# Kernel tuning notes

Measured on AMD Instinct MI355X. Metric: run time of the kernel, lower is better.

The kernel has to match this reference:

```python
import jax, jax.numpy as jnp
import numpy as np

B, N, M = 4, 1024, 3072          # batch, latent (query) len, prefix context len
D, H, DH, L, F = 512, 8, 64, 6, 2048  # dim, heads, dim_head, depth, ff hidden
SCALE = DH ** -0.5


def _ln(x, g, b):
    m = jnp.mean(x, axis=-1, keepdims=True)
    v = jnp.mean(jnp.square(x - m), axis=-1, keepdims=True)
    return (x - m) * jax.lax.rsqrt(v + 1e-5) * g + b


def _heads(t):  # [b, n, h*d] -> [b, h, n, d]
    b, n, _ = t.shape
    return t.reshape(b, n, H, DH).transpose(0, 2, 1, 3)


def _attend(q, k, v):
    # q:[b,h,i,d], k/v:[b,h,j,d]; causal mask triu(j-i+1) as in source
    i, j = q.shape[2], k.shape[2]
    sim = jnp.einsum('bhid,bhjd->bhij', q * SCALE, k)
    mask = jnp.triu(jnp.ones((i, j), dtype=bool), j - i + 1)
    sim = jnp.where(mask, -jnp.finfo(sim.dtype).max, sim)
    attn = jax.nn.softmax(sim, axis=-1)
    out = jnp.einsum('bhij,bhjd->bhid', attn, v)
    return out.transpose(0, 2, 1, 3).reshape(q.shape[0], i, H * DH)


def _ff(x, g, b, w1, w2):
    return jax.nn.gelu(_ln(x, g, b) @ w1, approximate=False) @ w2


def setup_inputs() -> dict:
    key = jax.random.key(0)
    ks = jax.random.split(key, 12)
    rn = lambda k, shape: jax.random.normal(k, shape, dtype=jnp.float32) * 0.02
    return {
        'x': jax.random.normal(ks[0], (B, N, D), jnp.float32),
        'context': jax.random.normal(ks[1], (B, M, D), jnp.float32),
        'pa_norm_g': jnp.ones((D,), jnp.float32), 'pa_norm_b': jnp.zeros((D,), jnp.float32),
        'pa_cnorm_g': jnp.ones((D,), jnp.float32), 'pa_cnorm_b': jnp.zeros((D,), jnp.float32),
        'pa_wq': rn(ks[2], (D, H * DH)), 'pa_wkv': rn(ks[3], (D, 2 * H * DH)),
        'pa_wo': rn(ks[4], (H * DH, D)), 'pa_wo_b': jnp.zeros((D,), jnp.float32),
        'pf_ln_g': jnp.ones((D,), jnp.float32), 'pf_ln_b': jnp.zeros((D,), jnp.float32),
        'pf_w1': rn(ks[5], (D, F)), 'pf_w2': rn(ks[6], (F, D)),
        'sa_ln_g': jnp.ones((L, D), jnp.float32), 'sa_ln_b': jnp.zeros((L, D), jnp.float32),
        'sa_wqkv': rn(ks[7], (L, D, 3 * H * DH)), 'sa_wo': rn(ks[8], (L, H * DH, D)),
        'sf_ln_g': jnp.ones((L, D), jnp.float32), 'sf_ln_b': jnp.zeros((L, D), jnp.float32),
        'sf_w1': rn(ks[9], (L, D, F)), 'sf_w2': rn(ks[10], (L, F, D)),
    }


def reference(x, context, pa_norm_g, pa_norm_b, pa_cnorm_g, pa_cnorm_b,
              pa_wq, pa_wkv, pa_wo, pa_wo_b, pf_ln_g, pf_ln_b, pf_w1, pf_w2,
              sa_ln_g, sa_ln_b, sa_wqkv, sa_wo, sf_ln_g, sf_ln_b, sf_w1, sf_w2):
    # --- CausalPrefixAttention (eval mode: no dropout, context_mask=None) ---
    xn = _ln(x, pa_norm_g, pa_norm_b)
    cn = _ln(context, pa_cnorm_g, pa_cnorm_b)
    q = _heads(xn @ pa_wq)
    k_in, v_in = jnp.split(xn @ pa_wkv, 2, axis=-1)
    k_c, v_c = jnp.split(cn @ pa_wkv, 2, axis=-1)
    k = _heads(jnp.concatenate([k_c, k_in], axis=1))  # [b,h,M+N,d]
    v = _heads(jnp.concatenate([v_c, v_in], axis=1))
    x = _attend(q, k, v) @ pa_wo + pa_wo_b + x
    x = _ff(x, pf_ln_g, pf_ln_b, pf_w1, pf_w2) + x
    # --- depth x (CausalAttention + FeedForward) ---
    for l in range(L):
        xn = _ln(x, sa_ln_g[l], sa_ln_b[l])
        qq, kk, vv = jnp.split(xn @ sa_wqkv[l], 3, axis=-1)
        x = _attend(_heads(qq), _heads(kk), _heads(vv)) @ sa_wo[l] + x
        x = _ff(x, sf_ln_g[l], sf_ln_b[l], sf_w1[l], sf_w2[l]) + x
    return x
```

## Files before the change

kernel.cpp:

```cpp
#include <hip/hip_runtime.h>
#include <hip/hip_bf16.h>
#include <cstdint>
#include <cstddef>

typedef __bf16 bf16;
typedef __attribute__((ext_vector_type(8))) __bf16 bf16x8;
typedef __attribute__((ext_vector_type(4))) __bf16 bf16x4;
typedef __attribute__((ext_vector_type(4))) float f32x4;

constexpr int B_ = 4, QN = 1024, MCTX = 3072, D_ = 512, H_ = 8, DHE = 64, L_ = 6, FF_ = 2048;
constexpr float SCL2_ = 0.18033688011f;

__device__ __forceinline__ f32x4 mfma16(bf16x8 a, bf16x8 b, f32x4 c) {
  return __builtin_amdgcn_mfma_f32_16x16x32_bf16(a, b, c, 0, 0, 0);
}

__device__ __forceinline__ void gl_lds16(const bf16* g, bf16* l) {
  __builtin_amdgcn_global_load_lds((const __attribute__((address_space(1))) void*)g,
                                   (__attribute__((address_space(3))) void*)l, 16, 0, 0);
}

__device__ __forceinline__ float fexp2(float x) {
  float r;
  asm("v_exp_f32 %0, %1" : "=v"(r) : "v"(x));
  return r;
}

__global__ __launch_bounds__(256) void ln_kernel(const float* __restrict__ x,
                                                 const float* __restrict__ g,
                                                 const float* __restrict__ b,
                                                 bf16* __restrict__ out, int rows) {
  int wid = threadIdx.x >> 6, lane = threadIdx.x & 63;
  int row = blockIdx.x * 4 + wid;
  if (row >= rows) return;
  const float* xr = x + (size_t)row * D_;
  f32x4 a0 = *(const f32x4*)(xr + lane * 8);
  f32x4 a1 = *(const f32x4*)(xr + lane * 8 + 4);
  float s = 0.f;
#pragma unroll
  for (int i = 0; i < 4; i++) { s += a0[i]; s += a1[i]; }
#pragma unroll
  for (int d = 1; d < 64; d <<= 1) s += __shfl_xor(s, d);
  float mean = s * (1.0f / 512.0f);
  float q = 0.f;
#pragma unroll
  for (int i = 0; i < 4; i++) {
    float t0 = a0[i] - mean, t1 = a1[i] - mean;
    q += t0 * t0 + t1 * t1;
  }
#pragma unroll
  for (int d = 1; d < 64; d <<= 1) q += __shfl_xor(q, d);
  float rstd = rsqrtf(q * (1.0f / 512.0f) + 1e-5f);
  f32x4 g0 = *(const f32x4*)(g + lane * 8);
  f32x4 g1 = *(const f32x4*)(g + lane * 8 + 4);
  f32x4 b0 = *(const f32x4*)(b + lane * 8);
  f32x4 b1 = *(const f32x4*)(b + lane * 8 + 4);
  bf16x8 o;
#pragma unroll
  for (int i = 0; i < 4; i++) {
    o[i] = (bf16)((a0[i] - mean) * rstd * g0[i] + b0[i]);
    o[i + 4] = (bf16)((a1[i] - mean) * rstd * g1[i] + b1[i]);
  }
  *(bf16x8*)(out + (size_t)row * D_ + lane * 8) = o;
}

struct WDesc { const float* src; bf16* dst; int K; int N; int tstart; };
struct WPack { WDesc d[30]; int n; };

__global__ __launch_bounds__(256) void wtrans_all(WPack p) {
  __shared__ float tile[64][65];
  const int bid = blockIdx.x;
  int mi = 0;
  for (int i = 1; i < p.n; i++)
    if (p.d[i].tstart <= bid) mi = i;
  const float* src = p.d[mi].src;
  bf16* dst = p.d[mi].dst;
  const int K = p.d[mi].K, N = p.d[mi].N;
  const int lt = bid - p.d[mi].tstart;
  const int ntx = N >> 6;
  const int n0 = (lt % ntx) * 64, k0 = (lt / ntx) * 64;
  const int tx = threadIdx.x, ty = threadIdx.y;
#pragma unroll
  for (int pp = 0; pp < 16; pp++)
    tile[pp * 4 + ty][tx] = src[(size_t)(k0 + pp * 4 + ty) * N + n0 + tx];
  __syncthreads();
#pragma unroll
  for (int pp = 0; pp < 16; pp++)
    dst[(size_t)(n0 + pp * 4 + ty) * K + k0 + tx] = (bf16)tile[tx][pp * 4 + ty];
}

template <int EPI>
__global__ __launch_bounds__(256) void gemm128(const bf16* __restrict__ A,
                                               const bf16* __restrict__ BT,
                                               void* __restrict__ C0,
                                               void* __restrict__ C1,
                                               void* __restrict__ C2,
                                               const float* __restrict__ resid,
                                               const float* __restrict__ bias,
                                               int M, int N, int K, int vstr) {
  __shared__ bf16 sm[6 * 4096];
  bf16* sA = sm;
  bf16* sB = sm + 3 * 4096;
  const int tid = threadIdx.x, wid = tid >> 6, lane = tid & 63;
  const int lr = lane & 15, lg = lane >> 4;
  const int tm = blockIdx.y * 128, tn = blockIdx.x * 128;
  const int wr = (wid >> 1) * 64, wc = (wid & 1) * 64;

  const int r0 = tid >> 2, ls0 = tid & 3;
  const int gs0 = ls0 ^ (r0 & 3);
  const bf16* gA0 = A + (size_t)(tm + r0) * K + gs0 * 8;
  const bf16* gB0 = BT + (size_t)(tn + r0) * K + gs0 * 8;
  const bf16* gA1 = gA0 + (size_t)64 * K;
  const bf16* gB1 = gB0 + (size_t)64 * K;

  f32x4 acc[4][4] = {};
  const int nt = K >> 5;

  auto stage = [&](int bi, int kt) {
    gl_lds16(gA0 + kt, sA + bi * 4096 + tid * 8);
    gl_lds16(gA1 + kt, sA + bi * 4096 + (tid + 256) * 8);
    gl_lds16(gB0 + kt, sB + bi * 4096 + tid * 8);
    gl_lds16(gB1 + kt, sB + bi * 4096 + (tid + 256) * 8);
  };

  stage(0, 0);
  stage(1, 32);

  for (int t = 0; t < nt; ++t) {
    const int bi = t % 3;
    if (t + 1 < nt) {
      asm volatile("s_waitcnt vmcnt(4)" ::: "memory");
    } else {
      asm volatile("s_waitcnt vmcnt(0)" ::: "memory");
    }
    __builtin_amdgcn_s_barrier();
    __builtin_amdgcn_sched_barrier(0);
    if (t + 2 < nt) stage((t + 2) % 3, (t + 2) * 32);

    bf16x8 af[4], bfr[4];
#pragma unroll
    for (int i = 0; i < 4; i++) {
      const int row = wr + i * 16 + lr;
      af[i] = *(const bf16x8*)&sA[bi * 4096 + row * 32 + ((lg ^ (row & 3)) * 8)];
    }
#pragma unroll
    for (int j = 0; j < 4; j++) {
      const int row = wc + j * 16 + lr;
      bfr[j] = *(const bf16x8*)&sB[bi * 4096 + row * 32 + ((lg ^ (row & 3)) * 8)];
    }
#pragma unroll
    for (int i = 0; i < 4; i++)
#pragma unroll
      for (int j = 0; j < 4; j++)
        acc[i][j] = mfma16(af[i], bfr[j], acc[i][j]);
  }

  const bool row_major_dst =
      (EPI == 1) || (EPI == 3 && tn < 1024) || (EPI == 4 && tn < 1024) || (EPI == 5 && tn < 512);
  if (row_major_dst) {
    bf16* dst;
    int dstr, rbase, coff;
    if (EPI == 1) { dst = (bf16*)C0; dstr = N; rbase = tm; coff = tn; }
    else if (EPI == 3) {
      if (tn < 512) { dst = (bf16*)C0; dstr = 512; rbase = tm; coff = tn; }
      else { dst = (bf16*)C1; dstr = 1024; rbase = (tm >> 10) * 4096 + (tm & 1023) + 3072; coff = tn - 512; }
    } else if (EPI == 4) { dst = (bf16*)C0; dstr = 1536; rbase = tm; coff = tn; }
    else { dst = (bf16*)C1; dstr = 1024; rbase = (tm / 3072) * 4096 + (tm % 3072); coff = tn; }

    __syncthreads();
    bf16* lb = sm;
#pragma unroll
    for (int i = 0; i < 4; i++) {
#pragma unroll
      for (int r = 0; r < 4; r++) {
        const int row = wr + i * 16 + lg * 4 + r;
#pragma unroll
        for (int j = 0; j < 4; j++) {
          const int col = wc + j * 16 + lr;
          float v = acc[i][j][r];
          if (EPI == 1) {
            float u = v * (0.7978845608f + 0.0356774081f * v * v);
            float e = fexp2(fminf(2.885390082f * u, 80.0f));
            v = v * e / (1.0f + e);
          }
          lb[row * 128 + (col ^ ((row & 7) << 3))] = (bf16)v;
        }
      }
    }
    __syncthreads();
#pragma unroll
    for (int p = 0; p < 8; p++) {
      const int row = p * 16 + (tid >> 4);
      const int cb = (tid & 15) * 8;
      bf16x8 v = *(const bf16x8*)&lb[row * 128 + (cb ^ ((row & 7) << 3))];
      *(bf16x8*)&dst[(size_t)(rbase + row) * dstr + coff + cb] = v;
    }
  } else {
#pragma unroll
    for (int i = 0; i < 4; i++) {
      const int row = tm + wr + i * 16 + lg * 4;
#pragma unroll
      for (int j = 0; j < 4; j++) {
        const int col = tn + wc + j * 16 + lr;
        bf16x4 pk = {(bf16)acc[i][j][0], (bf16)acc[i][j][1],
                     (bf16)acc[i][j][2], (bf16)acc[i][j][3]};
        if (EPI == 3) {
          const int cc = col - 1024, hh = cc >> 6, dh = cc & 63;
          const int bb = row >> 10, s = (row & 1023) + 3072;
          *(bf16x4*)&((bf16*)C2)[((size_t)(bb * 8 + hh) * 64 + dh) * vstr + s] = pk;
        } else if (EPI == 4) {
          const int cc = col - 1024, hh = cc >> 6, dh = cc & 63;
          const int bb = row >> 10, s = row & 1023;
          *(bf16x4*)&((bf16*)C2)[((size_t)(bb * 8 + hh) * 64 + dh) * vstr + s] = pk;
        } else {
          const int bq = row / 3072, s = row - bq * 3072;
          const int cc = col - 512, hh = cc >> 6, dh = cc & 63;
          *(bf16x4*)&((bf16*)C2)[((size_t)(bq * 8 + hh) * 64 + dh) * vstr + s] = pk;
        }
      }
    }
  }
}

__global__ __launch_bounds__(512) void gemm64k2(const bf16* __restrict__ A,
                                                const bf16* __restrict__ BT,
                                                float* __restrict__ Cout,
                                                const float* __restrict__ resid,
                                                const float* __restrict__ bias,
                                                int M, int N, int K) {
  __shared__ bf16 sm[3][2][64 * 64];
  const int tid = threadIdx.x, wid = tid >> 6, lane = tid & 63;
  const int lr = lane & 15, lg = lane >> 4;
  const int tm = blockIdx.y * 64, tn = blockIdx.x * 64;
  const int ws = wid >> 2;
  const int wq = wid & 3;
  const int wr = (wq >> 1) * 32, wc = (wq & 1) * 32;

  const int r0 = tid >> 3, u0 = tid & 7;
  const int g0 = u0 ^ (r0 & 7);
  const bf16* gA0 = A + (size_t)(tm + r0) * K + g0 * 8;
  const bf16* gB0 = BT + (size_t)(tn + r0) * K + g0 * 8;

  auto stage = [&](int bi, int kt) {
    gl_lds16(gA0 + kt, &sm[bi][0][tid * 8]);
    gl_lds16(gB0 + kt, &sm[bi][1][tid * 8]);
  };

  f32x4 acc[2][2] = {};
  const int nt = K >> 6;
  stage(0, 0);
  if (nt > 1) stage(1, 64);

  for (int t = 0; t < nt; ++t) {
    const int bi = t % 3;
    if (t + 1 < nt) {
      asm volatile("s_waitcnt vmcnt(2)" ::: "memory");
    } else {
      asm volatile("s_waitcnt vmcnt(0)" ::: "memory");
    }
    __builtin_amdgcn_s_barrier();
    __builtin_amdgcn_sched_barrier(0);
    if (t + 2 < nt) stage((t + 2) % 3, (t + 2) * 64);

    bf16x8 af[2], bfr[2];
#pragma unroll
    for (int i = 0; i < 2; i++) {
      const int row = wr + i * 16 + lr;
      af[i] = *(const bf16x8*)&sm[bi][0][row * 64 + (((ws * 4 + lg) ^ (row & 7)) * 8)];
    }
#pragma unroll
    for (int j = 0; j < 2; j++) {
      const int row = wc + j * 16 + lr;
      bfr[j] = *(const bf16x8*)&sm[bi][1][row * 64 + (((ws * 4 + lg) ^ (row & 7)) * 8)];
    }
#pragma unroll
    for (int i = 0; i < 2; i++)
#pragma unroll
      for (int j = 0; j < 2; j++)
        acc[i][j] = mfma16(af[i], bfr[j], acc[i][j]);
  }

  __syncthreads();
  float* lbuf = (float*)&sm[0][0][0];
  if (ws == 0) {
#pragma unroll
    for (int i = 0; i < 2; i++)
#pragma unroll
      for (int r = 0; r < 4; r++) {
        const int row = wr + i * 16 + lg * 4 + r;
#pragma unroll
        for (int j = 0; j < 2; j++)
          lbuf[row * 68 + wc + j * 16 + lr] = acc[i][j][r];
      }
  }
  __syncthreads();
  if (ws == 1) {
#pragma unroll
    for (int i = 0; i < 2; i++)
#pragma unroll
      for (int r = 0; r < 4; r++) {
        const int row = wr + i * 16 + lg * 4 + r;
#pragma unroll
        for (int j = 0; j < 2; j++)
          lbuf[row * 68 + wc + j * 16 + lr] += acc[i][j][r];
      }
  }
  __syncthreads();
#pragma unroll
  for (int p = 0; p < 2; p++) {
    const int row = p * 32 + (tid >> 4);
    const int col = (tid & 15) * 4;
    f32x4 v = *(const f32x4*)&lbuf[row * 68 + col];
    const size_t gidx = (size_t)(tm + row) * N + tn + col;
    f32x4 rs = *(const f32x4*)&resid[gidx];
    if (bias) {
      f32x4 bs = *(const f32x4*)&bias[tn + col];
#pragma unroll
      for (int e = 0; e < 4; e++) v[e] += bs[e];
    }
#pragma unroll
    for (int e = 0; e < 4; e++) v[e] += rs[e];
    *(f32x4*)&Cout[gidx] = v;
  }
}

template <int NSPLIT>
__global__ __launch_bounds__(512) void attn_kernel(const bf16* __restrict__ q, int qstride,
                                                   const bf16* __restrict__ k, int kstride,
                                                   const bf16* __restrict__ vt,
                                                   bf16* __restrict__ out,
                                                   bf16* __restrict__ po,
                                                   float* __restrict__ pm,
                                                   float* __restrict__ pl,
                                                   int Skv, int Moff, int spllen) {
  __shared__ bf16 kls[2][4096];
  __shared__ bf16 vls[2][4096];
  __shared__ bf16 pls[8][1024];

  const int tid = threadIdx.x, wid = tid >> 6, lane = tid & 63;
  const int lr = lane & 15, lg = lane >> 4, lg4 = lg * 4;
  const int b = blockIdx.z, h = blockIdx.y;
  const int qblk = blockIdx.x / NSPLIT;
  const int split = blockIdx.x % NSPLIT;
  const int q0b = qblk * 128;
  const int q0w = q0b + wid * 16;
  const int kv_lo = split * spllen;

  int jhi_blk = Moff + q0b + 127;
  if (jhi_blk > Skv - 1) jhi_blk = Skv - 1;
  int hi = kv_lo + spllen;
  if (hi > jhi_blk + 1) hi = jhi_blk + 1;
  const int ntl = (hi > kv_lo) ? ((hi - kv_lo + 63) >> 6) : 0;

  if (NSPLIT > 1 && ntl == 0) {
    size_t rb = ((size_t)split * B_ * H_ + (size_t)b * H_ + h) * QN + q0w;
    const int row = lane >> 2;
    bf16x8 z = {};
#pragma unroll
    for (int half = 0; half < 2; half++)
      *(bf16x8*)&po[(rb + row) * 64 + (lane & 3) * 16 + half * 8] = z;
    if (lg == 0) { pm[rb + lr] = -3e38f; pl[rb + lr] = 0.f; }
    return;
  }

  const int sel = ((tid >> 6) & 1) * 32 + ((tid >> 4) & 3) * 8;
  const int srow0 = (tid >> 7) * 16 + (tid & 15);
  const bf16* kbase = k + (size_t)b * Skv * kstride + h * DHE + sel;
  const bf16* vbase = vt + (size_t)((b * H_ + h) * DHE) * Skv + sel;

  const bf16* qp = q + (size_t)(b * QN + q0w + lr) * qstride + h * DHE;
  bf16x8 qa0 = *(const bf16x8*)(qp + lg * 8);
  bf16x8 qa1 = *(const bf16x8*)(qp + 32 + lg * 8);
#pragma unroll
  for (int i = 0; i < 8; i++) {
    qa0[i] = (bf16)((float)qa0[i] * SCL2_);
    qa1[i] = (bf16)((float)qa1[i] * SCL2_);
  }
  bf16x8 vones;
#pragma unroll
  for (int i = 0; i < 8; i++) vones[i] = (bf16)1.0f;

  f32x4 o[4] = {};
  f32x4 o4 = {};

  auto stage = [&](int bi, int j0) {
    gl_lds16(kbase + (size_t)(j0 + srow0) * kstride, &kls[bi][tid * 8]);
    gl_lds16(vbase + (size_t)srow0 * Skv + j0, &vls[bi][tid * 8]);
  };

  stage(0, kv_lo);
  __syncthreads();
  int buf = 0;
  bf16* pw = &pls[wid][0];

  for (int t = 0; t < ntl; ++t) {
    const int j0 = kv_lo + t * 64;
    if (t + 1 < ntl) stage(buf ^ 1, j0 + 64);
    const bf16* kbp = &kls[buf][0];
    const bf16* vbp = &vls[buf][0];

    f32x4 sv[4];
    __builtin_amdgcn_s_setprio(1);
#pragma unroll
    for (int kg = 0; kg < 4; kg++) {
      bf16x8 k0 = *(const bf16x8*)(kbp + (kg * 128 + lane) * 8);
      bf16x8 k1 = *(const bf16x8*)(kbp + (kg * 128 + 64 + lane) * 8);
      f32x4 z = {0.f, 0.f, 0.f, 0.f};
      z = mfma16(k0, qa0, z);
      z = mfma16(k1, qa1, z);
      sv[kg] = z;
    }
    __builtin_amdgcn_s_setprio(0);
    const bool full = (j0 + 63 <= Moff + q0w);
    if (!full) {
      const int limq = Moff + q0w + lr;
#pragma unroll
      for (int kg = 0; kg < 4; kg++)
#pragma unroll
        for (int r = 0; r < 4; r++)
          if (j0 + kg * 16 + lg4 + r > limq) sv[kg][r] = -3e38f;
    }
#pragma unroll
    for (int kg = 0; kg < 4; kg++) {
      float p0 = fexp2(sv[kg][0]);
      float p1 = fexp2(sv[kg][1]);
      float p2 = fexp2(sv[kg][2]);
      float p3 = fexp2(sv[kg][3]);
      bf16x4 pk = {(bf16)p0, (bf16)p1, (bf16)p2, (bf16)p3};
      const int k8 = kg * 2 + (lg >> 1);
      *(bf16x4*)(pw + ((k8 >> 2) * 64 + (k8 & 3) * 16 + lr) * 8 + (lg & 1) * 4) = pk;
    }
    bf16x8 pa0 = *(const bf16x8*)(pw + lane * 8);
    bf16x8 pa1 = *(const bf16x8*)(pw + (64 + lane) * 8);
    __builtin_amdgcn_s_setprio(1);
#pragma unroll
    for (int f = 0; f < 4; f++) {
      bf16x8 v0 = *(const bf16x8*)(vbp + (f * 128 + lane) * 8);
      bf16x8 v1 = *(const bf16x8*)(vbp + (f * 128 + 64 + lane) * 8);
      o[f] = mfma16(pa0, v0, o[f]);
      o[f] = mfma16(pa1, v1, o[f]);
    }
    o4 = mfma16(pa0, vones, o4);
    o4 = mfma16(pa1, vones, o4);
    __builtin_amdgcn_s_setprio(0);
    __syncthreads();
    buf ^= 1;
  }

  if (NSPLIT == 1) {
    float li[4];
#pragma unroll
    for (int r = 0; r < 4; r++) li[r] = 1.0f / o4[r];
#pragma unroll
    for (int f = 0; f < 4; f++)
#pragma unroll
      for (int r = 0; r < 4; r++) {
        const int row = lg4 + r, col = f * 16 + lr;
        pw[row * 64 + (col ^ ((row & 7) << 3))] = (bf16)(o[f][r] * li[r]);
      }
    const int row = lane >> 2;
#pragma unroll
    for (int half = 0; half < 2; half++) {
      const int cb = (lane & 3) * 16 + half * 8;
      bf16x8 v = *(const bf16x8*)&pw[row * 64 + (cb ^ ((row & 7) << 3))];
      *(bf16x8*)&out[(size_t)(b * QN + q0w + row) * D_ + h * DHE + cb] = v;
    }
  } else {
    size_t rb = ((size_t)split * B_ * H_ + (size_t)b * H_ + h) * QN + q0w;
#pragma unroll
    for (int f = 0; f < 4; f++)
#pragma unroll
      for (int r = 0; r < 4; r++) {
        const int row = lg4 + r, col = f * 16 + lr;
        pw[row * 64 + (col ^ ((row & 7) << 3))] = (bf16)o[f][r];
      }
    const int row = lane >> 2;
#pragma unroll
    for (int half = 0; half < 2; half++) {
      const int cb = (lane & 3) * 16 + half * 8;
      bf16x8 v = *(const bf16x8*)&pw[row * 64 + (cb ^ ((row & 7) << 3))];
      *(bf16x8*)&po[(rb + row) * 64 + cb] = v;
    }
    if (lr == 0) {
#pragma unroll
      for (int r = 0; r < 4; r++) {
        pm[rb + lg4 + r] = 0.f;
        pl[rb + lg4 + r] = o4[r];
      }
    }
  }
}

template <int NSPLIT>
__global__ __launch_bounds__(256) void attn_combine(const bf16* __restrict__ po,
                                                    const float* __restrict__ pm,
                                                    const float* __restrict__ pl,
                                                    bf16* __restrict__ out) {
  constexpr int TOT = B_ * H_ * QN;
  const int wid = threadIdx.x >> 6, lane = threadIdx.x & 63;
  const int row = blockIdx.x * 4 + wid;
  float mv[NSPLIT], lv[NSPLIT];
  float mstar = -3e38f;
#pragma unroll
  for (int s = 0; s < NSPLIT; s++) {
    mv[s] = pm[s * TOT + row];
    lv[s] = pl[s * TOT + row];
    mstar = fmaxf(mstar, mv[s]);
  }
  float lstar = 0.f, acc = 0.f;
#pragma unroll
  for (int s = 0; s < NSPLIT; s++) {
    float w = fexp2(mv[s] - mstar);
    lstar += lv[s] * w;
    acc += (float)po[((size_t)s * TOT + row) * 64 + lane] * w;
  }
  const int b = row >> 13, hq = row & 8191, h = hq >> 10, qq = hq & 1023;
  out[((size_t)b * QN + qq) * D_ + h * DHE + lane] = (bf16)(acc / lstar);
}

extern "C" void kernel_launch(void* const* d_in, const int* in_sizes, int n_in,
                              void* d_out, int out_size, void* d_ws, size_t ws_size,
                              hipStream_t stream) {
  const float* x       = (const float*)d_in[0];
  const float* ctx     = (const float*)d_in[1];
  const float* pa_ng   = (const float*)d_in[2];
  const float* pa_nb   = (const float*)d_in[3];
  const float* pa_cg   = (const float*)d_in[4];
  const float* pa_cb   = (const float*)d_in[5];
  const float* pa_wq   = (const float*)d_in[6];
  const float* pa_wkv  = (const float*)d_in[7];
  const float* pa_wo   = (const float*)d_in[8];
  const float* pa_wob  = (const float*)d_in[9];
  const float* pf_g    = (const float*)d_in[10];
  const float* pf_b    = (const float*)d_in[11];
  const float* pf_w1   = (const float*)d_in[12];
  const float* pf_w2   = (const float*)d_in[13];
  const float* sa_g    = (const float*)d_in[14];
  const float* sa_b    = (const float*)d_in[15];
  const float* sa_wqkv = (const float*)d_in[16];
  const float* sa_wo   = (const float*)d_in[17];
  const float* sf_g    = (const float*)d_in[18];
  const float* sf_b    = (const float*)d_in[19];
  const float* sf_w1   = (const float*)d_in[20];
  const float* sf_w2   = (const float*)d_in[21];
  float* xo = (float*)d_out;

  char* ws = (char*)d_ws;
  size_t off = 0;
  auto alloc = [&](size_t bytes) -> char* {
    char* p = ws + off;
    off += (bytes + 255) & ~(size_t)255;
    return p;
  };

  bf16* wqT    = (bf16*)alloc((size_t)512 * 512 * 2);
  bf16* wkvT   = (bf16*)alloc((size_t)1024 * 512 * 2);
  bf16* woT    = (bf16*)alloc((size_t)512 * 512 * 2);
  bf16* w1T    = (bf16*)alloc((size_t)2048 * 512 * 2);
  bf16* w2T    = (bf16*)alloc((size_t)512 * 2048 * 2);
  bf16* saqkvT = (bf16*)alloc((size_t)L_ * 1536 * 512 * 2);
  bf16* sawoT  = (bf16*)alloc((size_t)L_ * 512 * 512 * 2);
  bf16* sfw1T  = (bf16*)alloc((size_t)L_ * 2048 * 512 * 2);
  bf16* sfw2T  = (bf16*)alloc((size_t)L_ * 512 * 2048 * 2);
  bf16* xn    = (bf16*)alloc((size_t)4096 * 512 * 2);
  bf16* reg1  = (bf16*)alloc((size_t)12288 * 512 * 2);
  bf16* qb    = (bf16*)alloc((size_t)4096 * 512 * 2);
  bf16* reg2  = (bf16*)alloc((size_t)B_ * 4096 * 1024 * 2);
  bf16* vtb   = (bf16*)alloc((size_t)B_ * H_ * 64 * 4096 * 2);
  bf16* attnb = (bf16*)alloc((size_t)4096 * 512 * 2);
  constexpr int NSPL = 4;
  constexpr int TOTR = B_ * H_ * QN;
  bf16* po = (bf16*)alloc((size_t)NSPL * TOTR * 64 * 2);
  float* pmb = (float*)alloc((size_t)NSPL * TOTR * 4);
  float* plb = (float*)alloc((size_t)NSPL * TOTR * 4);
  const bool use_split = (off <= ws_size);
  bf16* cn = reg1;
  bf16* qkvb = reg1;
  bf16* kvb = reg2;
  bf16* ffh = reg2;
  (void)in_sizes; (void)n_in; (void)out_size;

  WPack wp;
  int nt_acc = 0, wi = 0;
  auto addw = [&](const float* s, bf16* d, int K, int N) {
    wp.d[wi].src = s; wp.d[wi].dst = d; wp.d[wi].K = K; wp.d[wi].N = N;
    wp.d[wi].tstart = nt_acc;
    nt_acc += (N / 64) * (K / 64);
    wi++;
  };
  addw(pa_wq, wqT, 512, 512);
  addw(pa_wkv, wkvT, 512, 1024);
  addw(pa_wo, woT, 512, 512);
  addw(pf_w1, w1T, 512, 2048);
  addw(pf_w2, w2T, 2048, 512);
  for (int l = 0; l < L_; l++) {
    addw(sa_wqkv + (size_t)l * 512 * 1536, saqkvT + (size_t)l * 1536 * 512, 512, 1536);
    addw(sa_wo + (size_t)l * 512 * 512, sawoT + (size_t)l * 512 * 512, 512, 512);
    addw(sf_w1 + (size_t)l * 512 * 2048, sfw1T + (size_t)l * 2048 * 512, 512, 2048);
    addw(sf_w2 + (size_t)l * 2048 * 512, sfw2T + (size_t)l * 512 * 2048, 2048, 512);
  }
  wp.n = wi;
  wtrans_all<<<nt_acc, dim3(64, 4, 1), 0, stream>>>(wp);

  ln_kernel<<<1024, 256, 0, stream>>>(x, pa_ng, pa_nb, xn, 4096);
  ln_kernel<<<3072, 256, 0, stream>>>(ctx, pa_cg, pa_cb, cn, 12288);
  hipLaunchKernelGGL(HIP_KERNEL_NAME(gemm128<5>), dim3(1024 / 128, 12288 / 128), dim3(256), 0,
                     stream, cn, wkvT, nullptr, kvb, vtb, nullptr, nullptr, 12288, 1024, 512, 4096);
  hipLaunchKernelGGL(HIP_KERNEL_NAME(gemm128<3>), dim3(1536 / 128, 4096 / 128), dim3(256), 0,
                     stream, xn, wqT, qb, kvb, vtb, nullptr, nullptr, 4096, 1536, 512, 4096);
  if (use_split) {
    hipLaunchKernelGGL(HIP_KERNEL_NAME(attn_kernel<NSPL>), dim3((QN / 128) * NSPL, H_, B_), dim3(512), 0,
                       stream, qb, 512, kvb, 1024, vtb, attnb, po, pmb, plb, 4096, MCTX, 1024);
    hipLaunchKernelGGL(HIP_KERNEL_NAME(attn_combine<NSPL>), dim3(TOTR / 4), dim3(256), 0,
                       stream, po, pmb, plb, attnb);
  } else {
    hipLaunchKernelGGL(HIP_KERNEL_NAME(attn_kernel<1>), dim3(QN / 128, H_, B_), dim3(512), 0,
                       stream, qb, 512, kvb, 1024, vtb, attnb, po, pmb, plb, 4096, MCTX, 4096);
  }
  gemm64k2<<<dim3(512 / 64, 4096 / 64), 512, 0, stream>>>(attnb, woT, xo, x, pa_wob, 4096, 512, 512);
  ln_kernel<<<1024, 256, 0, stream>>>(xo, pf_g, pf_b, xn, 4096);
  hipLaunchKernelGGL(HIP_KERNEL_NAME(gemm128<1>), dim3(2048 / 128, 4096 / 128), dim3(256), 0,
                     stream, xn, w1T, ffh, nullptr, nullptr, nullptr, nullptr, 4096, 2048, 512, 0);
  gemm64k2<<<dim3(512 / 64, 4096 / 64), 512, 0, stream>>>(ffh, w2T, xo, xo, nullptr, 4096, 512, 2048);

  for (int l = 0; l < L_; l++) {
    ln_kernel<<<1024, 256, 0, stream>>>(xo, sa_g + l * 512, sa_b + l * 512, xn, 4096);
    hipLaunchKernelGGL(HIP_KERNEL_NAME(gemm128<4>), dim3(1536 / 128, 4096 / 128), dim3(256), 0,
                       stream, xn, saqkvT + (size_t)l * 1536 * 512, qkvb, nullptr, vtb,
                       nullptr, nullptr, 4096, 1536, 512, 1024);
    if (use_split) {
      hipLaunchKernelGGL(HIP_KERNEL_NAME(attn_kernel<2>), dim3((QN / 128) * 2, H_, B_), dim3(512), 0,
                         stream, qkvb, 1536, qkvb + 512, 1536, vtb, attnb, po, pmb, plb, 1024, 0, 512);
      hipLaunchKernelGGL(HIP_KERNEL_NAME(attn_combine<2>), dim3(TOTR / 4), dim3(256), 0,
                         stream, po, pmb, plb, attnb);
    } else {
      hipLaunchKernelGGL(HIP_KERNEL_NAME(attn_kernel<1>), dim3(QN / 128, H_, B_), dim3(512), 0,
                         stream, qkvb, 1536, qkvb + 512, 1536, vtb, attnb, po, pmb, plb, 1024, 0, 1024);
    }
    gemm64k2<<<dim3(512 / 64, 4096 / 64), 512, 0, stream>>>(attnb, sawoT + (size_t)l * 512 * 512,
                                                            xo, xo, nullptr, 4096, 512, 512);
    ln_kernel<<<1024, 256, 0, stream>>>(xo, sf_g + l * 512, sf_b + l * 512, xn, 4096);
    hipLaunchKernelGGL(HIP_KERNEL_NAME(gemm128<1>), dim3(2048 / 128, 4096 / 128), dim3(256), 0,
                       stream, xn, sfw1T + (size_t)l * 2048 * 512, ffh, nullptr, nullptr,
                       nullptr, nullptr, 4096, 2048, 512, 0);
    gemm64k2<<<dim3(512 / 64, 4096 / 64), 512, 0, stream>>>(ffh, sfw2T + (size_t)l * 512 * 2048,
                                                            xo, xo, nullptr, 4096, 512, 2048);
  }
}
```

Measured before the change: 754.5 us.

## Fuse split-attention combine into output projection GEMM and merge initial layernorms

Removes the separate attn_combine kernel by having the Wo projection GEMM read the split partial outputs and row sums directly, summing and normalizing them while staging its A operand into LDS. The max-tracking buffer is dropped, which relies on each split already using a common offset so that its partial sums can simply be added. The two initial layernorm launches are also merged into one kernel. The fused GEMM trades the async global-to-LDS triple-buffered pipeline for register loads with double buffering and extra arithmetic per tile, and it reads NSPL times more A data.

```diff
diff --git a/kernel.cpp b/kernel.cpp
--- a/kernel.cpp
+++ b/kernel.cpp
@@ -24,6 +24,38 @@
   float r;
   asm("v_exp_f32 %0, %1" : "=v"(r) : "v"(x));
   return r;
+}
+
+__device__ __forceinline__ void ln_row(const float* xr, const float* g, const float* b,
+                                       bf16* outr, int lane) {
+  f32x4 a0 = *(const f32x4*)(xr + lane * 8);
+  f32x4 a1 = *(const f32x4*)(xr + lane * 8 + 4);
+  float s = 0.f;
+#pragma unroll
+  for (int i = 0; i < 4; i++) { s += a0[i]; s += a1[i]; }
+#pragma unroll
+  for (int d = 1; d < 64; d <<= 1) s += __shfl_xor(s, d);
+  float mean = s * (1.0f / 512.0f);
+  float q = 0.f;
+#pragma unroll
+  for (int i = 0; i < 4; i++) {
+    float t0 = a0[i] - mean, t1 = a1[i] - mean;
+    q += t0 * t0 + t1 * t1;
+  }
+#pragma unroll
+  for (int d = 1; d < 64; d <<= 1) q += __shfl_xor(q, d);
+  float rstd = rsqrtf(q * (1.0f / 512.0f) + 1e-5f);
+  f32x4 g0 = *(const f32x4*)(g + lane * 8);
+  f32x4 g1 = *(const f32x4*)(g + lane * 8 + 4);
+  f32x4 b0 = *(const f32x4*)(b + lane * 8);
+  f32x4 b1 = *(const f32x4*)(b + lane * 8 + 4);
+  bf16x8 o;
+#pragma unroll
+  for (int i = 0; i < 4; i++) {
+    o[i] = (bf16)((a0[i] - mean) * rstd * g0[i] + b0[i]);
+    o[i + 4] = (bf16)((a1[i] - mean) * rstd * g1[i] + b1[i]);
+  }
+  *(bf16x8*)(outr + lane * 8) = o;
 }
 
 __global__ __launch_bounds__(256) void ln_kernel(const float* __restrict__ x,
@@ -33,35 +65,26 @@
   int wid = threadIdx.x >> 6, lane = threadIdx.x & 63;
   int row = blockIdx.x * 4 + wid;
   if (row >= rows) return;
-  const float* xr = x + (size_t)row * D_;
-  f32x4 a0 = *(const f32x4*)(xr + lane * 8);
-  f32x4 a1 = *(const f32x4*)(xr + lane * 8 + 4);
-  float s = 0.f;
-#pragma unroll
-  for (int i = 0; i < 4; i++) { s += a0[i]; s += a1[i]; }
-#pragma unroll
-  for (int d = 1; d < 64; d <<= 1) s += __shfl_xor(s, d);
-  float mean = s * (1.0f / 512.0f);
-  float q = 0.f;
-#pragma unroll
-  for (int i = 0; i < 4; i++) {
-    float t0 = a0[i] - mean, t1 = a1[i] - mean;
-    q += t0 * t0 + t1 * t1;
-  }
-#pragma unroll
-  for (int d = 1; d < 64; d <<= 1) q += __shfl_xor(q, d);
-  float rstd = rsqrtf(q * (1.0f / 512.0f) + 1e-5f);
-  f32x4 g0 = *(const f32x4*)(g + lane * 8);
-  f32x4 g1 = *(const f32x4*)(g + lane * 8 + 4);
-  f32x4 b0 = *(const f32x4*)(b + lane * 8);
-  f32x4 b1 = *(const f32x4*)(b + lane * 8 + 4);
-  bf16x8 o;
-#pragma unroll
-  for (int i = 0; i < 4; i++) {
-    o[i] = (bf16)((a0[i] - mean) * rstd * g0[i] + b0[i]);
-    o[i + 4] = (bf16)((a1[i] - mean) * rstd * g1[i] + b1[i]);
-  }
-  *(bf16x8*)(out + (size_t)row * D_ + lane * 8) = o;
+  ln_row(x + (size_t)row * D_, g, b, out + (size_t)row * D_, lane);
+}
+
+__global__ __launch_bounds__(256) void ln2_kernel(const float* __restrict__ xa,
+                                                  const float* __restrict__ ga,
+                                                  const float* __restrict__ ba,
+                                                  bf16* __restrict__ oa, int rowsa,
+                                                  const float* __restrict__ xb,
+                                                  const float* __restrict__ gb,
+                                                  const float* __restrict__ bb,
+                                                  bf16* __restrict__ ob, int rowsb) {
+  int wid = threadIdx.x >> 6, lane = threadIdx.x & 63;
+  int row = blockIdx.x * 4 + wid;
+  if (row < rowsa) {
+    ln_row(xa + (size_t)row * D_, ga, ba, oa + (size_t)row * D_, lane);
+  } else {
+    int r2 = row - rowsa;
+    if (r2 >= rowsb) return;
+    ln_row(xb + (size_t)r2 * D_, gb, bb, ob + (size_t)r2 * D_, lane);
+  }
 }
 
 struct WDesc { const float* src; bf16* dst; int K; int N; int tstart; };
@@ -222,11 +245,14 @@
   }
 }
 
+template <int NSPL>
 __global__ __launch_bounds__(512) void gemm64k2(const bf16* __restrict__ A,
                                                 const bf16* __restrict__ BT,
                                                 float* __restrict__ Cout,
                                                 const float* __restrict__ resid,
                                                 const float* __restrict__ bias,
+                                                const bf16* __restrict__ po,
+                                                const float* __restrict__ pl,
                                                 int M, int N, int K) {
   __shared__ bf16 sm[3][2][64 * 64];
   const int tid = threadIdx.x, wid = tid >> 6, lane = tid & 63;
@@ -235,33 +261,16 @@
   const int ws = wid >> 2;
   const int wq = wid & 3;
   const int wr = (wq >> 1) * 32, wc = (wq & 1) * 32;
+  constexpr int TOT = B_ * H_ * QN;
 
   const int r0 = tid >> 3, u0 = tid & 7;
   const int g0 = u0 ^ (r0 & 7);
-  const bf16* gA0 = A + (size_t)(tm + r0) * K + g0 * 8;
   const bf16* gB0 = BT + (size_t)(tn + r0) * K + g0 * 8;
-
-  auto stage = [&](int bi, int kt) {
-    gl_lds16(gA0 + kt, &sm[bi][0][tid * 8]);
-    gl_lds16(gB0 + kt, &sm[bi][1][tid * 8]);
-  };
 
   f32x4 acc[2][2] = {};
   const int nt = K >> 6;
-  stage(0, 0);
-  if (nt > 1) stage(1, 64);
-
-  for (int t = 0; t < nt; ++t) {
-    const int bi = t % 3;
-    if (t + 1 < nt) {
-      asm volatile("s_waitcnt vmcnt(2)" ::: "memory");
-    } else {
-      asm volatile("s_waitcnt vmcnt(0)" ::: "memory");
-    }
-    __builtin_amdgcn_s_barrier();
-    __builtin_amdgcn_sched_barrier(0);
-    if (t + 2 < nt) stage((t + 2) % 3, (t + 2) * 64);
-
+
+  auto domfma = [&](int bi) {
     bf16x8 af[2], bfr[2];
 #pragma unroll
     for (int i = 0; i < 2; i++) {
@@ -278,6 +287,73 @@
 #pragma unroll
       for (int j = 0; j < 2; j++)
         acc[i][j] = mfma16(af[i], bfr[j], acc[i][j]);
+  };
+
+  if (NSPL == 1) {
+    const bf16* gA0 = A + (size_t)(tm + r0) * K + g0 * 8;
+    auto stage = [&](int bi, int kt) {
+      gl_lds16(gA0 + kt, &sm[bi][0][tid * 8]);
+      gl_lds16(gB0 + kt, &sm[bi][1][tid * 8]);
+    };
+    stage(0, 0);
+    if (nt > 1) stage(1, 64);
+    for (int t = 0; t < nt; ++t) {
+      const int bi = t % 3;
+      if (t + 1 < nt) {
+        asm volatile("s_waitcnt vmcnt(2)" ::: "memory");
+      } else {
+        asm volatile("s_waitcnt vmcnt(0)" ::: "memory");
+      }
+      __builtin_amdgcn_s_barrier();
+      __builtin_amdgcn_sched_barrier(0);
+      if (t + 2 < nt) stage((t + 2) % 3, (t + 2) * 64);
+      domfma(bi);
+    }
+  } else {
+    const int rowA = tm + r0;
+    const int bb = rowA >> 10, qq = rowA & 1023;
+    bf16x8 pv[NSPL];
+    float lv[NSPL];
+    auto loadA = [&](int kt) {
+      const int k = kt + g0 * 8;
+      const int h = k >> 6, dh0 = k & 63;
+      const size_t pr = (size_t)(bb * H_ + h) * QN + qq;
+#pragma unroll
+      for (int s = 0; s < NSPL; s++) {
+        lv[s] = pl[(size_t)s * TOT + pr];
+        pv[s] = *(const bf16x8*)&po[((size_t)s * TOT + pr) * 64 + dh0];
+      }
+    };
+    auto writeA = [&](int bi) {
+      float l = 0.f;
+#pragma unroll
+      for (int s = 0; s < NSPL; s++) l += lv[s];
+      const float inv = 1.0f / l;
+      float a[8] = {};
+#pragma unroll
+      for (int s = 0; s < NSPL; s++)
+#pragma unroll
+        for (int j = 0; j < 8; j++) a[j] += (float)pv[s][j];
+      bf16x8 w;
+#pragma unroll
+      for (int j = 0; j < 8; j++) w[j] = (bf16)(a[j] * inv);
+      *(bf16x8*)&sm[bi][0][tid * 8] = w;
+    };
+    loadA(0);
+    gl_lds16(gB0, &sm[0][1][tid * 8]);
+    writeA(0);
+    __syncthreads();
+    int buf = 0;
+    for (int t = 0; t < nt; ++t) {
+      if (t + 1 < nt) {
+        loadA((t + 1) * 64);
+        gl_lds16(gB0 + (t + 1) * 64, &sm[buf ^ 1][1][tid * 8]);
+      }
+      domfma(buf);
+      if (t + 1 < nt) writeA(buf ^ 1);
+      __syncthreads();
+      buf ^= 1;
+    }
   }
 
   __syncthreads();
@@ -330,7 +406,6 @@
                                                    const bf16* __restrict__ vt,
                                                    bf16* __restrict__ out,
                                                    bf16* __restrict__ po,
-                                                   float* __restrict__ pm,
                                                    float* __restrict__ pl,
                                                    int Skv, int Moff, int spllen) {
   __shared__ bf16 kls[2][4096];
@@ -359,7 +434,7 @@
 #pragma unroll
     for (int half = 0; half < 2; half++)
       *(bf16x8*)&po[(rb + row) * 64 + (lane & 3) * 16 + half * 8] = z;
-    if (lg == 0) { pm[rb + lr] = -3e38f; pl[rb + lr] = 0.f; }
+    if (lg == 0) pl[rb + lr] = 0.f;
     return;
   }
 
@@ -483,39 +558,9 @@
     }
     if (lr == 0) {
 #pragma unroll
-      for (int r = 0; r < 4; r++) {
-        pm[rb + lg4 + r] = 0.f;
-        pl[rb + lg4 + r] = o4[r];
-      }
-    }
-  }
-}
-
-template <int NSPLIT>
-__global__ __launch_bounds__(256) void attn_combine(const bf16* __restrict__ po,
-                                                    const float* __restrict__ pm,
-                                                    const float* __restrict__ pl,
-                                                    bf16* __restrict__ out) {
-  constexpr int TOT = B_ * H_ * QN;
-  const int wid = threadIdx.x >> 6, lane = threadIdx.x & 63;
-  const int row = blockIdx.x * 4 + wid;
-  float mv[NSPLIT], lv[NSPLIT];
-  float mstar = -3e38f;
-#pragma unroll
-  for (int s = 0; s < NSPLIT; s++) {
-    mv[s] = pm[s * TOT + row];
-    lv[s] = pl[s * TOT + row];
-    mstar = fmaxf(mstar, mv[s]);
-  }
-  float lstar = 0.f, acc = 0.f;
-#pragma unroll
-  for (int s = 0; s < NSPLIT; s++) {
-    float w = fexp2(mv[s] - mstar);
-    lstar += lv[s] * w;
-    acc += (float)po[((size_t)s * TOT + row) * 64 + lane] * w;
-  }
-  const int b = row >> 13, hq = row & 8191, h = hq >> 10, qq = hq & 1023;
-  out[((size_t)b * QN + qq) * D_ + h * DHE + lane] = (bf16)(acc / lstar);
+      for (int r = 0; r < 4; r++) pl[rb + lg4 + r] = o4[r];
+    }
+  }
 }
 
 extern "C" void kernel_launch(void* const* d_in, const int* in_sizes, int n_in,
@@ -571,7 +616,6 @@
   constexpr int NSPL = 4;
   constexpr int TOTR = B_ * H_ * QN;
   bf16* po = (bf16*)alloc((size_t)NSPL * TOTR * 64 * 2);
-  float* pmb = (float*)alloc((size_t)NSPL * TOTR * 4);
   float* plb = (float*)alloc((size_t)NSPL * TOTR * 4);
   const bool use_split = (off <= ws_size);
   bf16* cn = reg1;
@@ -602,26 +646,30 @@
   wp.n = wi;
   wtrans_all<<<nt_acc, dim3(64, 4, 1), 0, stream>>>(wp);
 
-  ln_kernel<<<1024, 256, 0, stream>>>(x, pa_ng, pa_nb, xn, 4096);
-  ln_kernel<<<3072, 256, 0, stream>>>(ctx, pa_cg, pa_cb, cn, 12288);
+  ln2_kernel<<<4096, 256, 0, stream>>>(x, pa_ng, pa_nb, xn, 4096,
+                                       ctx, pa_cg, pa_cb, cn, 12288);
   hipLaunchKernelGGL(HIP_KERNEL_NAME(gemm128<5>), dim3(1024 / 128, 12288 / 128), dim3(256), 0,
                      stream, cn, wkvT, nullptr, kvb, vtb, nullptr, nullptr, 12288, 1024, 512, 4096);
   hipLaunchKernelGGL(HIP_KERNEL_NAME(gemm128<3>), dim3(1536 / 128, 4096 / 128), dim3(256), 0,
                      stream, xn, wqT, qb, kvb, vtb, nullptr, nullptr, 4096, 1536, 512, 4096);
   if (use_split) {
     hipLaunchKernelGGL(HIP_KERNEL_NAME(attn_kernel<NSPL>), dim3((QN / 128) * NSPL, H_, B_), dim3(512), 0,
-                       stream, qb, 512, kvb, 1024, vtb, attnb, po, pmb, plb, 4096, MCTX, 1024);
-    hipLaunchKernelGGL(HIP_KERNEL_NAME(attn_combine<NSPL>), dim3(TOTR / 4), dim3(256), 0,
-                       stream, po, pmb, plb, attnb);
+                       stream, qb, 512, kvb, 1024, vtb, attnb, po, plb, 4096, MCTX, 1024);
+    hipLaunchKernelGGL(HIP_KERNEL_NAME(gemm64k2<NSPL>), dim3(512 / 64, 4096 / 64), dim3(512), 0,
+                       stream, (const bf16*)nullptr, woT, xo, x, pa_wob, po, plb, 4096, 512, 512);
   } else {
     hipLaunchKernelGGL(HIP_KERNEL_NAME(attn_kernel<1>), dim3(QN / 128, H_, B_), dim3(512), 0,
-                       stream, qb, 512, kvb, 1024, vtb, attnb, po, pmb, plb, 4096, MCTX, 4096);
-  }
-  gemm64k2<<<dim3(512 / 64, 4096 / 64), 512, 0, stream>>>(attnb, woT, xo, x, pa_wob, 4096, 512, 512);
+                       stream, qb, 512, kvb, 1024, vtb, attnb, po, plb, 4096, MCTX, 4096);
+    hipLaunchKernelGGL(HIP_KERNEL_NAME(gemm64k2<1>), dim3(512 / 64, 4096 / 64), dim3(512), 0,
+                       stream, attnb, woT, xo, x, pa_wob, (const bf16*)nullptr, (const float*)nullptr,
+                       4096, 512, 512);
+  }
   ln_kernel<<<1024, 256, 0, stream>>>(xo, pf_g, pf_b, xn, 4096);
   hipLaunchKernelGGL(HIP_KERNEL_NAME(gemm128<1>), dim3(2048 / 128, 4096 / 128), dim3(256), 0,
                      stream, xn, w1T, ffh, nullptr, nullptr, nullptr, nullptr, 4096, 2048, 512, 0);
-  gemm64k2<<<dim3(512 / 64, 4096 / 64), 512, 0, stream>>>(ffh, w2T, xo, xo, nullptr, 4096, 512, 2048);
+  hipLaunchKernelGGL(HIP_KERNEL_NAME(gemm64k2<1>), dim3(512 / 64, 4096 / 64), dim3(512), 0,
+                     stream, ffh, w2T, xo, xo, (const float*)nullptr, (const bf16*)nullptr,
+                     (const float*)nullptr, 4096, 512, 2048);
 
   for (int l = 0; l < L_; l++) {
     ln_kernel<<<1024, 256, 0, stream>>>(xo, sa_g + l * 512, sa_b + l * 512, xn, 4096);
@@ -630,20 +678,24 @@
                        nullptr, nullptr, 4096, 1536, 512, 1024);
     if (use_split) {
       hipLaunchKernelGGL(HIP_KERNEL_NAME(attn_kernel<2>), dim3((QN / 128) * 2, H_, B_), dim3(512), 0,
-                         stream, qkvb, 1536, qkvb + 512, 1536, vtb, attnb, po, pmb, plb, 1024, 0, 512);
-      hipLaunchKernelGGL(HIP_KERNEL_NAME(attn_combine<2>), dim3(TOTR / 4), dim3(256), 0,
-                         stream, po, pmb, plb, attnb);
+                         stream, qkvb, 1536, qkvb + 512, 1536, vtb, attnb, po, plb, 1024, 0, 512);
+      hipLaunchKernelGGL(HIP_KERNEL_NAME(gemm64k2<2>), dim3(512 / 64, 4096 / 64), dim3(512), 0,
+                         stream, (const bf16*)nullptr, sawoT + (size_t)l * 512 * 512, xo, xo,
+                         (const float*)nullptr, po, plb, 4096, 512, 512);
     } else {
       hipLaunchKernelGGL(HIP_KERNEL_NAME(attn_kernel<1>), dim3(QN / 128, H_, B_), dim3(512), 0,
-                         stream, qkvb, 1536, qkvb + 512, 1536, vtb, attnb, po, pmb, plb, 1024, 0, 1024);
-    }
-    gemm64k2<<<dim3(512 / 64, 4096 / 64), 512, 0, stream>>>(attnb, sawoT + (size_t)l * 512 * 512,
-                                                            xo, xo, nullptr, 4096, 512, 512);
+                         stream, qkvb, 1536, qkvb + 512, 1536, vtb, attnb, po, plb, 1024, 0, 1024);
+      hipLaunchKernelGGL(HIP_KERNEL_NAME(gemm64k2<1>), dim3(512 / 64, 4096 / 64), dim3(512), 0,
+                         stream, attnb, sawoT + (size_t)l * 512 * 512, xo, xo,
+                         (const float*)nullptr, (const bf16*)nullptr, (const float*)nullptr,
+                         4096, 512, 512);
+    }
     ln_kernel<<<1024, 256, 0, stream>>>(xo, sf_g + l * 512, sf_b + l * 512, xn, 4096);
     hipLaunchKernelGGL(HIP_KERNEL_NAME(gemm128<1>), dim3(2048 / 128, 4096 / 128), dim3(256), 0,
                        stream, xn, sfw1T + (size_t)l * 2048 * 512, ffh, nullptr, nullptr,
                        nullptr, nullptr, 4096, 2048, 512, 0);
-    gemm64k2<<<dim3(512 / 64, 4096 / 64), 512, 0, stream>>>(ffh, sfw2T + (size_t)l * 512 * 2048,
-                                                            xo, xo, nullptr, 4096, 512, 2048);
-  }
-}
+    hipLaunchKernelGGL(HIP_KERNEL_NAME(gemm64k2<1>), dim3(512 / 64, 4096 / 64), dim3(512), 0,
+                       stream, ffh, sfw2T + (size_t)l * 512 * 2048, xo, xo, (const float*)nullptr,
+                       (const bf16*)nullptr, (const float*)nullptr, 4096, 512, 2048);
+  }
+}
```

Result: no change. 760.4 us (+0.8%).
